# Kernel optimization log

Hardware: AMD Instinct MI355X
Metric: run time of the kernel (lower is better)

Reference implementation:

```python
import jax, jax.numpy as jnp
import numpy as np

DN = ('NCHW', 'OIHW', 'NCHW')

def conv3x3(x, w):
    return jax.lax.conv_general_dilated(x, w, (1, 1), ((1, 1), (1, 1)), dimension_numbers=DN)

def dsc(x, w1, w2):
    # DynamicSparseConv: per-sample per-channel softmax 3x3 depthwise kernel + residual
    B, C, H, W = x.shape
    pooled = x.mean(axis=(2, 3))                                  # [B, C] (AdaptiveAvgPool2d(1))
    h = jax.nn.gelu(pooled @ w1.T, approximate=False)             # [B, Cr] (1x1 conv == matmul)
    logits = (h @ w2.T).reshape(B, C, 9)                          # [B, C, 9]
    wk = jax.nn.softmax(logits, axis=2)
    # 3x3 patches: [B, C*9, H, W], feature dim ordered (C, kh, kw)
    patches = jax.lax.conv_general_dilated_patches(x, (3, 3), (1, 1), ((1, 1), (1, 1)))
    patches = patches.reshape(B, C, 9, H, W)
    out = jnp.einsum('bckhw,bck->bchw', patches, wk)
    return out + x

def pixel_shuffle(x, r):
    B, C, H, W = x.shape
    c = C // (r * r)
    return x.reshape(B, c, r, r, H, W).transpose(0, 1, 4, 2, 5, 3).reshape(B, c, H * r, W * r)

def setup_inputs() -> dict:
    key = jax.random.key(0)
    ks = jax.random.split(key, 12)
    B, C, H, W, OUT = 16, 128, 64, 64, 64
    CR = max(4, C // 8)            # 16
    RE = max(4, OUT // 8)          # 8
    s = 0.05
    return {
        'x1': jax.random.normal(ks[0], (B, C, H, W), jnp.float32),
        'x2': jax.random.normal(ks[1], (B, C, H, W), jnp.float32),
        'd1_w1': jax.random.normal(ks[2], (CR, C), jnp.float32) * s,
        'd1_w2': jax.random.normal(ks[3], (9 * C, CR), jnp.float32) * s,
        'd2_w1': jax.random.normal(ks[4], (CR, C), jnp.float32) * s,
        'd2_w2': jax.random.normal(ks[5], (9 * C, CR), jnp.float32) * s,
        'align_w': jax.random.normal(ks[6], (C, 2 * C), jnp.float32) * s,
        'up_w1': jax.random.normal(ks[7], (4 * C, C, 3, 3), jnp.float32) * s,
        'up_w2': jax.random.normal(ks[8], (OUT, C), jnp.float32) * s,
        're_w1': jax.random.normal(ks[9], (RE, OUT, 3, 3), jnp.float32) * s,
        're_w2': jax.random.normal(ks[10], (OUT, RE, 3, 3), jnp.float32) * s,
    }

def reference(x1, x2, d1_w1, d1_w2, d2_w1, d2_w2, align_w, up_w1, up_w2, re_w1, re_w2):
    def dynamic_block(x):  # shared weights for both inputs (same nn.Sequential)
        x = dsc(x, d1_w1, d1_w2)
        x = jax.nn.relu(x)
        return dsc(x, d2_w1, d2_w2)
    a = dynamic_block(x1)
    b = dynamic_block(x2)
    fused = jnp.einsum('bchw,oc->bohw', jnp.concatenate([a, b], axis=1), align_w)  # 1x1 conv
    u = conv3x3(fused, up_w1)            # [B, 4C, H, W]
    u = pixel_shuffle(u, 2)              # [B, C, 2H, 2W]
    up = jnp.einsum('bchw,oc->bohw', u, up_w2)  # [B, OUT, 2H, 2W]
    re = conv3x3(jax.nn.relu(conv3x3(up, re_w1)), re_w2)
    return up + re
```

## Files before the change

### kernel.cpp

```cpp
#include <hip/hip_runtime.h>
#include <math.h>

typedef unsigned short ushort;
typedef short bf16x8 __attribute__((ext_vector_type(8)));
typedef float f32x16 __attribute__((ext_vector_type(16)));
typedef float f32x4 __attribute__((ext_vector_type(4)));

static const size_t OFF_POOLED = 0;
static const size_t OFF_WK     = 4096;
static const size_t OFF_WT     = 40960;
static const size_t OFF_WF     = 188416;
static const size_t OFF_AW1    = 204800;
static const size_t OFF_AW2    = 209408;
static const size_t OFF_T      = 262144;
static const size_t OFF_AB     = 8650752;
static const size_t OFF_F      = 17039360;

static __device__ __forceinline__ ushort f2bf(float f) {
    unsigned int u = __builtin_bit_cast(unsigned int, f);
    u += 0x7FFF + ((u >> 16) & 1);
    return (ushort)(u >> 16);
}
static __device__ __forceinline__ float bf2f(ushort u) {
    return __builtin_bit_cast(float, ((unsigned int)u) << 16);
}

__global__ __launch_bounds__(256) void pool_both_kernel(const float* __restrict__ x1,
                                                        const float* __restrict__ x2,
                                                        float* __restrict__ pooled) {
    int bc = blockIdx.x;
    const float* x = (bc >> 11) ? x2 : x1;
    const float4* p = (const float4*)(x + (size_t)(bc & 2047) * 4096);
    float s = 0.f;
    for (int i = threadIdx.x; i < 1024; i += 256) {
        float4 v = p[i];
        s += v.x + v.y + v.z + v.w;
    }
    #pragma unroll
    for (int off = 32; off; off >>= 1) s += __shfl_down(s, off);
    __shared__ float r4[4];
    if ((threadIdx.x & 63) == 0) r4[threadIdx.x >> 6] = s;
    __syncthreads();
    if (threadIdx.x == 0) pooled[bc] = (r4[0] + r4[1] + r4[2] + r4[3]) * (1.f / 4096.f);
}

__global__ __launch_bounds__(128) void wk_kernel(const float* __restrict__ pooled,
                                                 const float* __restrict__ w1,
                                                 const float* __restrict__ w2,
                                                 float* __restrict__ wk) {
    int b = blockIdx.x;
    __shared__ float sp[128];
    __shared__ float sh[16];
    int t = threadIdx.x;
    sp[t] = pooled[b * 128 + t];
    __syncthreads();
    if (t < 16) {
        float acc = 0.f;
        #pragma unroll 4
        for (int c = 0; c < 128; c++) acc += w1[t * 128 + c] * sp[c];
        sh[t] = 0.5f * acc * (1.f + erff(acc * 0.70710678118654752f));
    }
    __syncthreads();
    float lg[9];
    float m = -INFINITY;
    #pragma unroll
    for (int k = 0; k < 9; k++) {
        float acc = 0.f;
        const float* wr = w2 + (size_t)(t * 9 + k) * 16;
        #pragma unroll
        for (int r = 0; r < 16; r++) acc += wr[r] * sh[r];
        lg[k] = acc;
        m = fmaxf(m, acc);
    }
    float se = 0.f;
    #pragma unroll
    for (int k = 0; k < 9; k++) { lg[k] = expf(lg[k] - m); se += lg[k]; }
    float inv = 1.f / se;
    #pragma unroll
    for (int k = 0; k < 9; k++) wk[(size_t)(b * 128 + t) * 9 + k] = lg[k] * inv;
}

__global__ __launch_bounds__(256) void dsc1_kernel(const float* __restrict__ x1,
                                                   const float* __restrict__ x2,
                                                   const float* __restrict__ wk,
                                                   ushort* __restrict__ y,
                                                   float* __restrict__ pooled2) {
    int bc = blockIdx.x;
    const float* xp = ((bc >> 11) ? x2 : x1) + (size_t)(bc & 2047) * 4096;
    ushort* yp = y + (size_t)bc * 4096;
    __shared__ float tile[66 * 66];
    __shared__ float r4[4];
    int t = threadIdx.x;
    for (int i = t; i < 66 * 66; i += 256) tile[i] = 0.f;
    __syncthreads();
    const float4* xp4 = (const float4*)xp;
    for (int i = t; i < 1024; i += 256) {
        float4 v = xp4[i];
        int h = i >> 4, w = (i & 15) * 4;
        float* d = &tile[(h + 1) * 66 + w + 1];
        d[0] = v.x; d[1] = v.y; d[2] = v.z; d[3] = v.w;
    }
    __syncthreads();
    float kk[9];
    #pragma unroll
    for (int k = 0; k < 9; k++) kk[k] = wk[(size_t)bc * 9 + k];
    float psum = 0.f;
    for (int i = t * 2; i < 4096; i += 512) {
        int h = i >> 6, w = i & 63;
        const float* c = &tile[h * 66 + w];
        float v0 = kk[0]*c[0] + kk[1]*c[1] + kk[2]*c[2]
                 + kk[3]*c[66] + kk[4]*c[67] + kk[5]*c[68]
                 + kk[6]*c[132] + kk[7]*c[133] + kk[8]*c[134] + c[67];
        float v1 = kk[0]*c[1] + kk[1]*c[2] + kk[2]*c[3]
                 + kk[3]*c[67] + kk[4]*c[68] + kk[5]*c[69]
                 + kk[6]*c[133] + kk[7]*c[134] + kk[8]*c[135] + c[68];
        v0 = fmaxf(v0, 0.f); v1 = fmaxf(v1, 0.f);
        psum += v0 + v1;
        ushort2 pk = {f2bf(v0), f2bf(v1)};
        *(ushort2*)&yp[i] = pk;
    }
    #pragma unroll
    for (int off = 32; off; off >>= 1) psum += __shfl_down(psum, off);
    if ((t & 63) == 0) r4[t >> 6] = psum;
    __syncthreads();
    if (t == 0) pooled2[bc] = (r4[0] + r4[1] + r4[2] + r4[3]) * (1.f / 4096.f);
}

__global__ __launch_bounds__(256) void dsc2_kernel(const ushort* __restrict__ x,
                                                   const float* __restrict__ wk,
                                                   ushort* __restrict__ y) {
    int bc = blockIdx.x;
    const ushort* xp = x + (size_t)bc * 4096;
    ushort* yp = y + (size_t)bc * 4096;
    __shared__ float tile[66 * 66];
    int t = threadIdx.x;
    for (int i = t; i < 66 * 66; i += 256) tile[i] = 0.f;
    __syncthreads();
    for (int i = t; i < 512; i += 256) {
        int4 raw = *(const int4*)&xp[i * 8];
        const ushort* u = (const ushort*)&raw;
        int h = i >> 3, w = (i & 7) * 8;
        float* d = &tile[(h + 1) * 66 + w + 1];
        #pragma unroll
        for (int j = 0; j < 8; j++) d[j] = bf2f(u[j]);
    }
    __syncthreads();
    float kk[9];
    #pragma unroll
    for (int k = 0; k < 9; k++) kk[k] = wk[(size_t)bc * 9 + k];
    for (int i = t * 2; i < 4096; i += 512) {
        int h = i >> 6, w = i & 63;
        const float* c = &tile[h * 66 + w];
        float v0 = kk[0]*c[0] + kk[1]*c[1] + kk[2]*c[2]
                 + kk[3]*c[66] + kk[4]*c[67] + kk[5]*c[68]
                 + kk[6]*c[132] + kk[7]*c[133] + kk[8]*c[134] + c[67];
        float v1 = kk[0]*c[1] + kk[1]*c[2] + kk[2]*c[3]
                 + kk[3]*c[67] + kk[4]*c[68] + kk[5]*c[69]
                 + kk[6]*c[133] + kk[7]*c[134] + kk[8]*c[135] + c[68];
        ushort2 pk = {f2bf(v0), f2bf(v1)};
        *(ushort2*)&yp[i] = pk;
    }
}

__global__ __launch_bounds__(256) void awprep_kernel(const float* __restrict__ W,
                                                     ushort* __restrict__ Wf) {
    int t = threadIdx.x;
    #pragma unroll 1
    for (int i = 0; i < 16; i++) {
        int tk = t + (i << 8);
        int step = tk >> 8, mt = (tk >> 6) & 3, lane = tk & 63;
        int o = mt * 32 + (lane & 31);
        int cb = step * 16 + (lane >> 5) * 8;
        #pragma unroll
        for (int j = 0; j < 8; j++) Wf[(size_t)tk * 8 + j] = f2bf(W[o * 256 + cb + j]);
    }
}

__global__ __launch_bounds__(256, 2) void align_mfma_kernel(const ushort* __restrict__ A,
                                                            const ushort* __restrict__ Bv,
                                                            const ushort* __restrict__ Wf,
                                                            ushort* __restrict__ F) {
    __shared__ ushort Xs[2 * 128 * 8];
    const int b = blockIdx.y;
    const int px0 = blockIdx.x << 7;
    const int tid = threadIdx.x;
    const int wave = tid >> 6, lane = tid & 63;
    const int l31 = lane & 31, half = lane >> 5;

    f32x16 acc[4];
    #pragma unroll
    for (int mt = 0; mt < 4; mt++)
        #pragma unroll
        for (int r = 0; r < 16; r++) acc[mt][r] = 0.f;

    const int cg0 = tid >> 7, pxs0 = tid & 127;
    const int bfofs = (wave * 32 + l31) * 8 + half * 1024;

    for (int step = 0; step < 16; step++) {
        const ushort* src =
            (step < 8 ? A : Bv) + (((size_t)(b * 128 + (step & 7) * 16)) << 12) + px0;
        if (step) __syncthreads();
        #pragma unroll
        for (int q = 0; q < 2; q++) {
            int cg = cg0 + q * 2, px = pxs0;
            ushort v0 = src[((size_t)(cg * 4 + 0) << 12) + px];
            ushort v1 = src[((size_t)(cg * 4 + 1) << 12) + px];
            ushort v2 = src[((size_t)(cg * 4 + 2) << 12) + px];
            ushort v3 = src[((size_t)(cg * 4 + 3) << 12) + px];
            ushort4 pk = {v0, v1, v2, v3};
            *(ushort4*)&Xs[(cg >> 1) * 1024 + px * 8 + (cg & 1) * 4] = pk;
        }
        __syncthreads();
        bf16x8 bfrag = *(const bf16x8*)&Xs[bfofs];
        const bf16x8* wf = (const bf16x8*)(Wf + ((size_t)step * 4 * 64 + lane) * 8);
        #pragma unroll
        for (int mt = 0; mt < 4; mt++)
            acc[mt] = __builtin_amdgcn_mfma_f32_32x32x16_bf16(wf[mt * 64], bfrag, acc[mt], 0, 0, 0);
    }
    ushort* fp = F + ((size_t)(b * 4096 + px0 + wave * 32 + l31)) * 128;
    #pragma unroll
    for (int mt = 0; mt < 4; mt++) {
        #pragma unroll
        for (int g = 0; g < 4; g++) {
            ushort4 pk = {f2bf(acc[mt][g * 4 + 0]), f2bf(acc[mt][g * 4 + 1]),
                          f2bf(acc[mt][g * 4 + 2]), f2bf(acc[mt][g * 4 + 3])};
            *(ushort4*)(fp + mt * 32 + half * 4 + 8 * g) = pk;
        }
    }
}

__global__ __launch_bounds__(256) void wcomb_kernel(const float* __restrict__ w1,
                                                    const float* __restrict__ w2,
                                                    ushort* __restrict__ Awt) {
    int idx = blockIdx.x * 256 + threadIdx.x;
    int j = idx & 7;
    int lane = (idx >> 3) & 63;
    int mt = (idx >> 9) & 3;
    int mh = (idx >> 11) & 1;
    int s = idx >> 12;
    int tap = s >> 3, c16 = s & 7;
    int op = mh * 128 + mt * 32 + (lane & 31);
    int cin = c16 * 16 + (lane >> 5) * 8 + j;
    int o = op >> 2, ph = op & 3;
    float acc = 0.f;
    #pragma unroll 4
    for (int c = 0; c < 128; c++)
        acc += w2[o * 128 + c] * w1[((size_t)(c * 4 + ph) * 128 + cin) * 9 + tap];
    Awt[idx] = f2bf(acc);
}

__global__ __launch_bounds__(256) void aw1prep_kernel(const float* __restrict__ w1,
                                                      ushort* __restrict__ Aw1) {
    int idx = blockIdx.x * 256 + threadIdx.x;
    if (idx >= 9216) return;
    int j = idx & 7, lane = (idx >> 3) & 63, s = idx >> 9;
    int m = lane & 15, kq = lane >> 4;
    int tap = s >> 1, ch = s & 1;
    int cin = ch * 32 + kq * 8 + j;
    float v = (m < 8) ? w1[((size_t)(m * 64 + cin)) * 9 + tap] : 0.f;
    Aw1[idx] = f2bf(v);
}

__global__ __launch_bounds__(256) void aw2prep_kernel(const float* __restrict__ w2,
                                                      ushort* __restrict__ Aw2) {
    int idx = blockIdx.x * 256 + threadIdx.x;
    if (idx >= 5120) return;
    int j = idx & 7, lane = (idx >> 3) & 63, mt = (idx >> 9) & 1, s = idx >> 10;
    int m = mt * 32 + (lane & 31), half = lane >> 5;
    int k = s * 16 + half * 8 + j;
    int tap = k >> 3, c = k & 7;
    float v = (tap < 9) ? w2[((size_t)(m * 8 + c)) * 9 + tap] : 0.f;
    Aw2[idx] = f2bf(v);
}

__global__ __launch_bounds__(256, 2) void up_mfma_kernel(const ushort* __restrict__ F,
                                                         const ushort* __restrict__ Awt,
                                                         ushort* __restrict__ U) {
    __shared__ ushort Xs[180 * 136];
    const int b = blockIdx.y;
    const int tr = blockIdx.x >> 3, tc = blockIdx.x & 7;
    const int tid = threadIdx.x;
    const int wave = tid >> 6, lane = tid & 63;
    const int l31 = lane & 31, half = lane >> 5;
    const int mh = wave >> 1, nh = wave & 1;

    for (int idx = tid; idx < 2880; idx += 256) {
        int px = idx >> 4, q = idx & 15;
        int r = px / 10, c = px - r * 10;
        int gh = tr * 16 - 1 + r, gw = tc * 8 - 1 + c;
        int4 v = {0, 0, 0, 0};
        if ((unsigned)gh < 64u && (unsigned)gw < 64u)
            v = *(const int4*)(F + ((size_t)(b * 4096 + gh * 64 + gw)) * 128 + q * 8);
        *(int4*)&Xs[px * 136 + q * 8] = v;
    }
    __syncthreads();

    f32x16 acc[4][2];
    #pragma unroll
    for (int mt = 0; mt < 4; mt++)
        #pragma unroll
        for (int nt = 0; nt < 2; nt++)
            #pragma unroll
            for (int r = 0; r < 16; r++) acc[mt][nt][r] = 0.f;

    int xb[2];
    #pragma unroll
    for (int nt = 0; nt < 2; nt++) {
        int pxl = nh * 64 + nt * 32 + l31;
        xb[nt] = ((pxl >> 3) * 10 + (pxl & 7)) * 136 + half * 8;
    }

    const ushort* abase = Awt + (size_t)(mh * 4) * 512 + lane * 8;
    bf16x8 A0[4], A1[4], AN0[4], AN1[4];
    #pragma unroll
    for (int mt = 0; mt < 4; mt++) {
        A0[mt] = *(const bf16x8*)(abase + (size_t)mt * 512);
        A1[mt] = *(const bf16x8*)(abase + 4096 + (size_t)mt * 512);
    }

    #pragma unroll 1
    for (int s = 0; s < 72; s += 2) {
        if (s + 2 < 72) {
            #pragma unroll
            for (int mt = 0; mt < 4; mt++)
                AN0[mt] = *(const bf16x8*)(abase + (size_t)(s + 2) * 4096 + mt * 512);
        }
        {
            int tap = s >> 3, c16 = s & 7;
            int ky = tap / 3, kx = tap - ky * 3;
            int xoff = (ky * 10 + kx) * 136 + c16 * 16;
            bf16x8 b0 = *(const bf16x8*)&Xs[xb[0] + xoff];
            bf16x8 b1 = *(const bf16x8*)&Xs[xb[1] + xoff];
            #pragma unroll
            for (int mt = 0; mt < 4; mt++) {
                acc[mt][0] = __builtin_amdgcn_mfma_f32_32x32x16_bf16(A0[mt], b0, acc[mt][0], 0, 0, 0);
                acc[mt][1] = __builtin_amdgcn_mfma_f32_32x32x16_bf16(A0[mt], b1, acc[mt][1], 0, 0, 0);
            }
        }
        if (s + 3 < 72) {
            #pragma unroll
            for (int mt = 0; mt < 4; mt++)
                AN1[mt] = *(const bf16x8*)(abase + (size_t)(s + 3) * 4096 + mt * 512);
        }
        {
            int s1 = s + 1;
            int tap = s1 >> 3, c16 = s1 & 7;
            int ky = tap / 3, kx = tap - ky * 3;
            int xoff = (ky * 10 + kx) * 136 + c16 * 16;
            bf16x8 b0 = *(const bf16x8*)&Xs[xb[0] + xoff];
            bf16x8 b1 = *(const bf16x8*)&Xs[xb[1] + xoff];
            #pragma unroll
            for (int mt = 0; mt < 4; mt++) {
                acc[mt][0] = __builtin_amdgcn_mfma_f32_32x32x16_bf16(A1[mt], b0, acc[mt][0], 0, 0, 0);
                acc[mt][1] = __builtin_amdgcn_mfma_f32_32x32x16_bf16(A1[mt], b1, acc[mt][1], 0, 0, 0);
            }
        }
        #pragma unroll
        for (int mt = 0; mt < 4; mt++) { A0[mt] = AN0[mt]; A1[mt] = AN1[mt]; }
    }

    const int S2 = 68;
    #pragma unroll 1
    for (int p = 0; p < 2; p++) {
        __syncthreads();
        if (nh == p) {
            #pragma unroll
            for (int nt = 0; nt < 2; nt++) {
                int pxl = nh * 64 + nt * 32 + l31;
                int rowl = pxl >> 3, coll = pxl & 7;
                int Y0 = 2 * (rowl - 8 * p), X0 = 2 * coll;
                #pragma unroll
                for (int mt = 0; mt < 4; mt++) {
                    #pragma unroll
                    for (int g = 0; g < 4; g++) {
                        int o = mh * 32 + mt * 8 + 2 * g + half;
                        #pragma unroll
                        for (int i = 0; i < 4; i++) {
                            int ry = (i >> 1), rx = i & 1;
                            Xs[((Y0 + ry) * 16 + X0 + rx) * S2 + o] =
                                f2bf(acc[mt][nt][g * 4 + i]);
                        }
                    }
                }
            }
        }
        __syncthreads();
        for (int idx = tid; idx < 4096; idx += 256) {
            int px = idx >> 4, q = idx & 15;
            ushort4 v = *(ushort4*)&Xs[px * S2 + q * 4];
            int Yg = tr * 32 + p * 16 + (px >> 4), Xg = tc * 16 + (px & 15);
            *(ushort4*)(U + ((size_t)((b * 128 + Yg) * 128 + Xg)) * 64 + q * 4) = v;
        }
    }
}

__global__ __launch_bounds__(256, 2) void re1_kernel(const ushort* __restrict__ U,
                                                     const ushort* __restrict__ Aw1,
                                                     ushort* __restrict__ R1) {
    __shared__ ushort Xs[324 * 72];
    __shared__ ushort As[18 * 64 * 8];
    const int b = blockIdx.y;
    const int ty = blockIdx.x >> 3, tx = blockIdx.x & 7;
    const int tid = threadIdx.x;
    const int wave = tid >> 6, lane = tid & 63;
    const int m16 = lane & 15, kq = lane >> 4;

    for (int idx = tid; idx < 1152; idx += 256)
        *(int4*)&As[idx * 8] = *(const int4*)(Aw1 + (size_t)idx * 8);
    for (int idx = tid; idx < 2592; idx += 256) {
        int px = idx >> 3, q = idx & 7;
        int r = px / 18, c = px - r * 18;
        int gY = ty * 16 - 1 + r, gX = tx * 16 - 1 + c;
        int4 v = {0, 0, 0, 0};
        if ((unsigned)gY < 128u && (unsigned)gX < 128u)
            v = *(const int4*)(U + ((size_t)((b * 128 + gY) * 128 + gX)) * 64 + q * 8);
        *(int4*)&Xs[px * 72 + q * 8] = v;
    }
    __syncthreads();

    f32x4 acc[4];
    #pragma unroll
    for (int nt = 0; nt < 4; nt++)
        #pragma unroll
        for (int r = 0; r < 4; r++) acc[nt][r] = 0.f;

    #pragma unroll 1
    for (int s = 0; s < 18; s++) {
        bf16x8 a = *(const bf16x8*)&As[(s * 64 + lane) * 8];
        int tap = s >> 1, ch = s & 1;
        int ky = tap / 3, kx = tap - ky * 3;
        int xo = (ky * 18 + kx) * 72 + ch * 32 + kq * 8;
        #pragma unroll
        for (int nt = 0; nt < 4; nt++) {
            int row = wave * 4 + nt;
            bf16x8 bv = *(const bf16x8*)&Xs[(row * 18 + m16) * 72 + xo];
            acc[nt] = __builtin_amdgcn_mfma_f32_16x16x32_bf16(a, bv, acc[nt], 0, 0, 0);
        }
    }
    if (kq < 2) {
        #pragma unroll
        for (int nt = 0; nt < 4; nt++) {
            int gY = ty * 16 + wave * 4 + nt, gX = tx * 16 + m16;
            ushort4 pk = {f2bf(fmaxf(acc[nt][0], 0.f)), f2bf(fmaxf(acc[nt][1], 0.f)),
                          f2bf(fmaxf(acc[nt][2], 0.f)), f2bf(fmaxf(acc[nt][3], 0.f))};
            *(ushort4*)(R1 + ((size_t)((b * 128 + gY) * 128 + gX)) * 8 + kq * 4) = pk;
        }
    }
}

__global__ __launch_bounds__(256, 2) void re2_kernel(const ushort* __restrict__ R1,
                                                     const ushort* __restrict__ U,
                                                     const ushort* __restrict__ Aw2,
                                                     float* __restrict__ out) {
    __shared__ ushort Xs[324 * 8];
    __shared__ ushort As[5 * 2 * 64 * 8];
    __shared__ ushort Us[256 * 68];
    const int b = blockIdx.y;
    const int ty = blockIdx.x >> 3, tx = blockIdx.x & 7;
    const int tid = threadIdx.x;
    const int wave = tid >> 6, lane = tid & 63;
    const int l31 = lane & 31, half = lane >> 5;

    for (int idx = tid; idx < 640; idx += 256)
        *(int4*)&As[idx * 8] = *(const int4*)(Aw2 + (size_t)idx * 8);
    for (int idx = tid; idx < 324; idx += 256) {
        int r = idx / 18, c = idx - r * 18;
        int gY = ty * 16 - 1 + r, gX = tx * 16 - 1 + c;
        int4 v = {0, 0, 0, 0};
        if ((unsigned)gY < 128u && (unsigned)gX < 128u)
            v = *(const int4*)(R1 + ((size_t)((b * 128 + gY) * 128 + gX)) * 8);
        *(int4*)&Xs[idx * 8] = v;
    }
    for (int idx = tid; idx < 2048; idx += 256) {
        int px = idx >> 3, q = idx & 7;
        int gY = ty * 16 + (px >> 4), gX = tx * 16 + (px & 15);
        const ushort* s = U + ((size_t)((b * 128 + gY) * 128 + gX)) * 64 + q * 8;
        ushort4 v0 = *(const ushort4*)s;
        ushort4 v1 = *(const ushort4*)(s + 4);
        *(ushort4*)&Us[px * 68 + q * 8] = v0;
        *(ushort4*)&Us[px * 68 + q * 8 + 4] = v1;
    }
    __syncthreads();

    f32x16 acc[2][2];
    #pragma unroll
    for (int mt = 0; mt < 2; mt++)
        #pragma unroll
        for (int nt = 0; nt < 2; nt++)
            #pragma unroll
            for (int r = 0; r < 16; r++) acc[mt][nt][r] = 0.f;

    #pragma unroll
    for (int s = 0; s < 5; s++) {
        bf16x8 a0 = *(const bf16x8*)&As[((s * 2 + 0) * 64 + lane) * 8];
        bf16x8 a1 = *(const bf16x8*)&As[((s * 2 + 1) * 64 + lane) * 8];
        int t = 2 * s + half;
        if (t > 8) t = 8;
        int ky = t / 3, kx = t - ky * 3;
        #pragma unroll
        for (int nt = 0; nt < 2; nt++) {
            int pxl = wave * 64 + nt * 32 + l31;
            int row = pxl >> 4, col = pxl & 15;
            bf16x8 bv = *(const bf16x8*)&Xs[((row + ky) * 18 + col + kx) * 8];
            acc[0][nt] = __builtin_amdgcn_mfma_f32_32x32x16_bf16(a0, bv, acc[0][nt], 0, 0, 0);
            acc[1][nt] = __builtin_amdgcn_mfma_f32_32x32x16_bf16(a1, bv, acc[1][nt], 0, 0, 0);
        }
    }
    #pragma unroll
    for (int mt = 0; mt < 2; mt++) {
        #pragma unroll
        for (int nt = 0; nt < 2; nt++) {
            int pxl = wave * 64 + nt * 32 + l31;
            int gY = ty * 16 + (pxl >> 4), gX = tx * 16 + (pxl & 15);
            #pragma unroll
            for (int r = 0; r < 16; r++) {
                int o = mt * 32 + (r & 3) + 8 * (r >> 2) + 4 * half;
                float v = acc[mt][nt][r] + bf2f(Us[pxl * 68 + o]);
                out[((size_t)(b * 64 + o) * 128 + gY) * 128 + gX] = v;
            }
        }
    }
}

extern "C" void kernel_launch(void* const* d_in, const int* in_sizes, int n_in,
                              void* d_out, int out_size, void* d_ws, size_t ws_size,
                              hipStream_t stream) {
    const float* x1      = (const float*)d_in[0];
    const float* x2      = (const float*)d_in[1];
    const float* d1_w1   = (const float*)d_in[2];
    const float* d1_w2   = (const float*)d_in[3];
    const float* d2_w1   = (const float*)d_in[4];
    const float* d2_w2   = (const float*)d_in[5];
    const float* align_w = (const float*)d_in[6];
    const float* up_w1   = (const float*)d_in[7];
    const float* up_w2   = (const float*)d_in[8];
    const float* re_w1   = (const float*)d_in[9];
    const float* re_w2   = (const float*)d_in[10];
    float* out = (float*)d_out;
    float* ws  = (float*)d_ws;

    float*  pooled = ws + OFF_POOLED;
    float*  wkb    = ws + OFF_WK;
    ushort* Awt    = (ushort*)(ws + OFF_WT);
    ushort* Wf     = (ushort*)(ws + OFF_WF);
    ushort* Aw1    = (ushort*)(ws + OFF_AW1);
    ushort* Aw2    = (ushort*)(ws + OFF_AW2);
    ushort* bufT   = (ushort*)(ws + OFF_T);
    ushort* R1     = (ushort*)(ws + OFF_T);
    ushort* bufAB  = (ushort*)(ws + OFF_AB);
    ushort* bufU   = (ushort*)(ws + OFF_AB);
    ushort* F      = (ushort*)(ws + OFF_F);

    wcomb_kernel<<<1152, 256, 0, stream>>>(up_w1, up_w2, Awt);
    awprep_kernel<<<1, 256, 0, stream>>>(align_w, Wf);
    aw1prep_kernel<<<36, 256, 0, stream>>>(re_w1, Aw1);
    aw2prep_kernel<<<20, 256, 0, stream>>>(re_w2, Aw2);

    pool_both_kernel<<<4096, 256, 0, stream>>>(x1, x2, pooled);
    wk_kernel<<<32, 128, 0, stream>>>(pooled, d1_w1, d1_w2, wkb);
    dsc1_kernel<<<4096, 256, 0, stream>>>(x1, x2, wkb, bufT, pooled);
    wk_kernel<<<32, 128, 0, stream>>>(pooled, d2_w1, d2_w2, wkb);
    dsc2_kernel<<<4096, 256, 0, stream>>>(bufT, wkb, bufAB);

    align_mfma_kernel<<<dim3(32, 16), 256, 0, stream>>>(bufAB, bufAB + 8388608, Wf, F);
    up_mfma_kernel<<<dim3(32, 16), 256, 0, stream>>>(F, Awt, bufU);
    re1_kernel<<<dim3(64, 16), 256, 0, stream>>>(bufU, Aw1, R1);
    re2_kernel<<<dim3(64, 16), 256, 0, stream>>>(R1, bufU, Aw2, out);
}
```

Before: 359.5 us.

## Fuse dynamic-kernel computation into dsc kernels and split up-conv output channels

Removes the two small wk_kernel launches and instead recomputes, inside each dsc block, the gelu MLP hidden vector and that channel's 9 softmax weights from the pooled vector. The up_mfma kernel now splits its output channels across two blocks, doubling the grid. Each block holds half the accumulators and uses an XOR-swizzled unpadded LDS layout for the input tile, and the launch bound is raised to 3 blocks per CU. The cost is redundant per-block MLP work (16x128 dot products per block) and the input tile being loaded twice in the up conv.

Measured after the change: 368.0 us. 2.3% more time.

```diff
diff --git a/kernel.cpp b/kernel.cpp
--- a/kernel.cpp
+++ b/kernel.cpp
@@ -44,45 +44,11 @@
     if (threadIdx.x == 0) pooled[bc] = (r4[0] + r4[1] + r4[2] + r4[3]) * (1.f / 4096.f);
 }
 
-__global__ __launch_bounds__(128) void wk_kernel(const float* __restrict__ pooled,
-                                                 const float* __restrict__ w1,
-                                                 const float* __restrict__ w2,
-                                                 float* __restrict__ wk) {
-    int b = blockIdx.x;
-    __shared__ float sp[128];
-    __shared__ float sh[16];
-    int t = threadIdx.x;
-    sp[t] = pooled[b * 128 + t];
-    __syncthreads();
-    if (t < 16) {
-        float acc = 0.f;
-        #pragma unroll 4
-        for (int c = 0; c < 128; c++) acc += w1[t * 128 + c] * sp[c];
-        sh[t] = 0.5f * acc * (1.f + erff(acc * 0.70710678118654752f));
-    }
-    __syncthreads();
-    float lg[9];
-    float m = -INFINITY;
-    #pragma unroll
-    for (int k = 0; k < 9; k++) {
-        float acc = 0.f;
-        const float* wr = w2 + (size_t)(t * 9 + k) * 16;
-        #pragma unroll
-        for (int r = 0; r < 16; r++) acc += wr[r] * sh[r];
-        lg[k] = acc;
-        m = fmaxf(m, acc);
-    }
-    float se = 0.f;
-    #pragma unroll
-    for (int k = 0; k < 9; k++) { lg[k] = expf(lg[k] - m); se += lg[k]; }
-    float inv = 1.f / se;
-    #pragma unroll
-    for (int k = 0; k < 9; k++) wk[(size_t)(b * 128 + t) * 9 + k] = lg[k] * inv;
-}
-
 __global__ __launch_bounds__(256) void dsc1_kernel(const float* __restrict__ x1,
                                                    const float* __restrict__ x2,
-                                                   const float* __restrict__ wk,
+                                                   const float* __restrict__ pooled,
+                                                   const float* __restrict__ w1,
+                                                   const float* __restrict__ w2,
                                                    ushort* __restrict__ y,
                                                    float* __restrict__ pooled2) {
     int bc = blockIdx.x;
@@ -90,9 +56,19 @@
     ushort* yp = y + (size_t)bc * 4096;
     __shared__ float tile[66 * 66];
     __shared__ float r4[4];
+    __shared__ float sp[128];
+    __shared__ float sh[16];
+    __shared__ float lgs[9];
     int t = threadIdx.x;
+    if (t < 128) sp[t] = pooled[(bc >> 7) * 128 + t];
     for (int i = t; i < 66 * 66; i += 256) tile[i] = 0.f;
     __syncthreads();
+    if (t < 16) {
+        float a = 0.f;
+        #pragma unroll 4
+        for (int c = 0; c < 128; c++) a += w1[t * 128 + c] * sp[c];
+        sh[t] = 0.5f * a * (1.f + erff(a * 0.70710678118654752f));
+    }
     const float4* xp4 = (const float4*)xp;
     for (int i = t; i < 1024; i += 256) {
         float4 v = xp4[i];
@@ -101,9 +77,26 @@
         d[0] = v.x; d[1] = v.y; d[2] = v.z; d[3] = v.w;
     }
     __syncthreads();
+    if (t < 9) {
+        float a = 0.f;
+        const float* wr = w2 + (size_t)((bc & 127) * 9 + t) * 16;
+        #pragma unroll
+        for (int r = 0; r < 16; r++) a += wr[r] * sh[r];
+        lgs[t] = a;
+    }
+    __syncthreads();
     float kk[9];
-    #pragma unroll
-    for (int k = 0; k < 9; k++) kk[k] = wk[(size_t)bc * 9 + k];
+    {
+        float m = -INFINITY;
+        #pragma unroll
+        for (int k = 0; k < 9; k++) m = fmaxf(m, lgs[k]);
+        float se = 0.f;
+        #pragma unroll
+        for (int k = 0; k < 9; k++) { kk[k] = expf(lgs[k] - m); se += kk[k]; }
+        float inv = 1.f / se;
+        #pragma unroll
+        for (int k = 0; k < 9; k++) kk[k] *= inv;
+    }
     float psum = 0.f;
     for (int i = t * 2; i < 4096; i += 512) {
         int h = i >> 6, w = i & 63;
@@ -127,15 +120,27 @@
 }
 
 __global__ __launch_bounds__(256) void dsc2_kernel(const ushort* __restrict__ x,
-                                                   const float* __restrict__ wk,
+                                                   const float* __restrict__ pooled,
+                                                   const float* __restrict__ w1,
+                                                   const float* __restrict__ w2,
                                                    ushort* __restrict__ y) {
     int bc = blockIdx.x;
     const ushort* xp = x + (size_t)bc * 4096;
     ushort* yp = y + (size_t)bc * 4096;
     __shared__ float tile[66 * 66];
+    __shared__ float sp[128];
+    __shared__ float sh[16];
+    __shared__ float lgs[9];
     int t = threadIdx.x;
+    if (t < 128) sp[t] = pooled[(bc >> 7) * 128 + t];
     for (int i = t; i < 66 * 66; i += 256) tile[i] = 0.f;
     __syncthreads();
+    if (t < 16) {
+        float a = 0.f;
+        #pragma unroll 4
+        for (int c = 0; c < 128; c++) a += w1[t * 128 + c] * sp[c];
+        sh[t] = 0.5f * a * (1.f + erff(a * 0.70710678118654752f));
+    }
     for (int i = t; i < 512; i += 256) {
         int4 raw = *(const int4*)&xp[i * 8];
         const ushort* u = (const ushort*)&raw;
@@ -145,9 +150,26 @@
         for (int j = 0; j < 8; j++) d[j] = bf2f(u[j]);
     }
     __syncthreads();
+    if (t < 9) {
+        float a = 0.f;
+        const float* wr = w2 + (size_t)((bc & 127) * 9 + t) * 16;
+        #pragma unroll
+        for (int r = 0; r < 16; r++) a += wr[r] * sh[r];
+        lgs[t] = a;
+    }
+    __syncthreads();
     float kk[9];
-    #pragma unroll
-    for (int k = 0; k < 9; k++) kk[k] = wk[(size_t)bc * 9 + k];
+    {
+        float m = -INFINITY;
+        #pragma unroll
+        for (int k = 0; k < 9; k++) m = fmaxf(m, lgs[k]);
+        float se = 0.f;
+        #pragma unroll
+        for (int k = 0; k < 9; k++) { kk[k] = expf(lgs[k] - m); se += kk[k]; }
+        float inv = 1.f / se;
+        #pragma unroll
+        for (int k = 0; k < 9; k++) kk[k] *= inv;
+    }
     for (int i = t * 2; i < 4096; i += 512) {
         int h = i >> 6, w = i & 63;
         const float* c = &tile[h * 66 + w];
@@ -273,16 +295,18 @@
     Aw2[idx] = f2bf(v);
 }
 
-__global__ __launch_bounds__(256, 2) void up_mfma_kernel(const ushort* __restrict__ F,
+__global__ __launch_bounds__(256, 3) void up_mfma_kernel(const ushort* __restrict__ F,
                                                          const ushort* __restrict__ Awt,
                                                          ushort* __restrict__ U) {
-    __shared__ ushort Xs[180 * 136];
+    __shared__ ushort Xs[180 * 128];
     const int b = blockIdx.y;
-    const int tr = blockIdx.x >> 3, tc = blockIdx.x & 7;
+    const int oh = blockIdx.x & 1;
+    const int tile = blockIdx.x >> 1;
+    const int tr = tile >> 3, tc = tile & 7;
     const int tid = threadIdx.x;
     const int wave = tid >> 6, lane = tid & 63;
     const int l31 = lane & 31, half = lane >> 5;
-    const int mh = wave >> 1, nh = wave & 1;
+    const int mh2 = wave >> 1, nh = wave & 1;
 
     for (int idx = tid; idx < 2880; idx += 256) {
         int px = idx >> 4, q = idx & 15;
@@ -291,29 +315,29 @@
         int4 v = {0, 0, 0, 0};
         if ((unsigned)gh < 64u && (unsigned)gw < 64u)
             v = *(const int4*)(F + ((size_t)(b * 4096 + gh * 64 + gw)) * 128 + q * 8);
-        *(int4*)&Xs[px * 136 + q * 8] = v;
-    }
-    __syncthreads();
-
-    f32x16 acc[4][2];
-    #pragma unroll
-    for (int mt = 0; mt < 4; mt++)
+        *(int4*)&Xs[px * 128 + ((q ^ (px & 7)) << 3)] = v;
+    }
+    __syncthreads();
+
+    f32x16 acc[2][2];
+    #pragma unroll
+    for (int mt = 0; mt < 2; mt++)
         #pragma unroll
         for (int nt = 0; nt < 2; nt++)
             #pragma unroll
             for (int r = 0; r < 16; r++) acc[mt][nt][r] = 0.f;
 
-    int xb[2];
+    int xpos[2];
     #pragma unroll
     for (int nt = 0; nt < 2; nt++) {
         int pxl = nh * 64 + nt * 32 + l31;
-        xb[nt] = ((pxl >> 3) * 10 + (pxl & 7)) * 136 + half * 8;
-    }
-
-    const ushort* abase = Awt + (size_t)(mh * 4) * 512 + lane * 8;
-    bf16x8 A0[4], A1[4], AN0[4], AN1[4];
-    #pragma unroll
-    for (int mt = 0; mt < 4; mt++) {
+        xpos[nt] = (pxl >> 3) * 10 + (pxl & 7);
+    }
+
+    const ushort* abase = Awt + (size_t)(oh * 4 + mh2 * 2) * 512 + lane * 8;
+    bf16x8 A0[2], A1[2], AN0[2], AN1[2];
+    #pragma unroll
+    for (int mt = 0; mt < 2; mt++) {
         A0[mt] = *(const bf16x8*)(abase + (size_t)mt * 512);
         A1[mt] = *(const bf16x8*)(abase + 4096 + (size_t)mt * 512);
     }
@@ -322,44 +346,48 @@
     for (int s = 0; s < 72; s += 2) {
         if (s + 2 < 72) {
             #pragma unroll
-            for (int mt = 0; mt < 4; mt++)
+            for (int mt = 0; mt < 2; mt++)
                 AN0[mt] = *(const bf16x8*)(abase + (size_t)(s + 2) * 4096 + mt * 512);
         }
         {
             int tap = s >> 3, c16 = s & 7;
             int ky = tap / 3, kx = tap - ky * 3;
-            int xoff = (ky * 10 + kx) * 136 + c16 * 16;
-            bf16x8 b0 = *(const bf16x8*)&Xs[xb[0] + xoff];
-            bf16x8 b1 = *(const bf16x8*)&Xs[xb[1] + xoff];
-            #pragma unroll
-            for (int mt = 0; mt < 4; mt++) {
+            int koff = ky * 10 + kx;
+            int qq = c16 * 2 + half;
+            int p0 = xpos[0] + koff, p1 = xpos[1] + koff;
+            bf16x8 b0 = *(const bf16x8*)&Xs[p0 * 128 + ((qq ^ (p0 & 7)) << 3)];
+            bf16x8 b1 = *(const bf16x8*)&Xs[p1 * 128 + ((qq ^ (p1 & 7)) << 3)];
+            #pragma unroll
+            for (int mt = 0; mt < 2; mt++) {
                 acc[mt][0] = __builtin_amdgcn_mfma_f32_32x32x16_bf16(A0[mt], b0, acc[mt][0], 0, 0, 0);
                 acc[mt][1] = __builtin_amdgcn_mfma_f32_32x32x16_bf16(A0[mt], b1, acc[mt][1], 0, 0, 0);
             }
         }
         if (s + 3 < 72) {
             #pragma unroll
-            for (int mt = 0; mt < 4; mt++)
+            for (int mt = 0; mt < 2; mt++)
                 AN1[mt] = *(const bf16x8*)(abase + (size_t)(s + 3) * 4096 + mt * 512);
         }
         {
             int s1 = s + 1;
             int tap = s1 >> 3, c16 = s1 & 7;
             int ky = tap / 3, kx = tap - ky * 3;
-            int xoff = (ky * 10 + kx) * 136 + c16 * 16;
-            bf16x8 b0 = *(const bf16x8*)&Xs[xb[0] + xoff];
-            bf16x8 b1 = *(const bf16x8*)&Xs[xb[1] + xoff];
-            #pragma unroll
-            for (int mt = 0; mt < 4; mt++) {
+            int koff = ky * 10 + kx;
+            int qq = c16 * 2 + half;
+            int p0 = xpos[0] + koff, p1 = xpos[1] + koff;
+            bf16x8 b0 = *(const bf16x8*)&Xs[p0 * 128 + ((qq ^ (p0 & 7)) << 3)];
+            bf16x8 b1 = *(const bf16x8*)&Xs[p1 * 128 + ((qq ^ (p1 & 7)) << 3)];
+            #pragma unroll
+            for (int mt = 0; mt < 2; mt++) {
                 acc[mt][0] = __builtin_amdgcn_mfma_f32_32x32x16_bf16(A1[mt], b0, acc[mt][0], 0, 0, 0);
                 acc[mt][1] = __builtin_amdgcn_mfma_f32_32x32x16_bf16(A1[mt], b1, acc[mt][1], 0, 0, 0);
             }
         }
         #pragma unroll
-        for (int mt = 0; mt < 4; mt++) { A0[mt] = AN0[mt]; A1[mt] = AN1[mt]; }
-    }
-
-    const int S2 = 68;
+        for (int mt = 0; mt < 2; mt++) { A0[mt] = AN0[mt]; A1[mt] = AN1[mt]; }
+    }
+
+    const int S2 = 36;
     #pragma unroll 1
     for (int p = 0; p < 2; p++) {
         __syncthreads();
@@ -370,10 +398,10 @@
                 int rowl = pxl >> 3, coll = pxl & 7;
                 int Y0 = 2 * (rowl - 8 * p), X0 = 2 * coll;
                 #pragma unroll
-                for (int mt = 0; mt < 4; mt++) {
+                for (int mt = 0; mt < 2; mt++) {
                     #pragma unroll
                     for (int g = 0; g < 4; g++) {
-                        int o = mh * 32 + mt * 8 + 2 * g + half;
+                        int o = mh2 * 16 + mt * 8 + 2 * g + half;
                         #pragma unroll
                         for (int i = 0; i < 4; i++) {
                             int ry = (i >> 1), rx = i & 1;
@@ -385,11 +413,11 @@
             }
         }
         __syncthreads();
-        for (int idx = tid; idx < 4096; idx += 256) {
-            int px = idx >> 4, q = idx & 15;
+        for (int idx = tid; idx < 2048; idx += 256) {
+            int px = idx >> 3, q = idx & 7;
             ushort4 v = *(ushort4*)&Xs[px * S2 + q * 4];
             int Yg = tr * 32 + p * 16 + (px >> 4), Xg = tc * 16 + (px & 15);
-            *(ushort4*)(U + ((size_t)((b * 128 + Yg) * 128 + Xg)) * 64 + q * 4) = v;
+            *(ushort4*)(U + ((size_t)((b * 128 + Yg) * 128 + Xg)) * 64 + oh * 32 + q * 4) = v;
         }
     }
 }
@@ -539,8 +567,8 @@
     float* out = (float*)d_out;
     float* ws  = (float*)d_ws;
 
-    float*  pooled = ws + OFF_POOLED;
-    float*  wkb    = ws + OFF_WK;
+    float*  pooled  = ws + OFF_POOLED;
+    float*  pooled2 = ws + OFF_WK;
     ushort* Awt    = (ushort*)(ws + OFF_WT);
     ushort* Wf     = (ushort*)(ws + OFF_WF);
     ushort* Aw1    = (ushort*)(ws + OFF_AW1);
@@ -557,13 +585,11 @@
     aw2prep_kernel<<<20, 256, 0, stream>>>(re_w2, Aw2);
 
     pool_both_kernel<<<4096, 256, 0, stream>>>(x1, x2, pooled);
-    wk_kernel<<<32, 128, 0, stream>>>(pooled, d1_w1, d1_w2, wkb);
-    dsc1_kernel<<<4096, 256, 0, stream>>>(x1, x2, wkb, bufT, pooled);
-    wk_kernel<<<32, 128, 0, stream>>>(pooled, d2_w1, d2_w2, wkb);
-    dsc2_kernel<<<4096, 256, 0, stream>>>(bufT, wkb, bufAB);
+    dsc1_kernel<<<4096, 256, 0, stream>>>(x1, x2, pooled, d1_w1, d1_w2, bufT, pooled2);
+    dsc2_kernel<<<4096, 256, 0, stream>>>(bufT, pooled2, d2_w1, d2_w2, bufAB);
 
     align_mfma_kernel<<<dim3(32, 16), 256, 0, stream>>>(bufAB, bufAB + 8388608, Wf, F);
-    up_mfma_kernel<<<dim3(32, 16), 256, 0, stream>>>(F, Awt, bufU);
+    up_mfma_kernel<<<dim3(64, 16), 256, 0, stream>>>(F, Awt, bufU);
     re1_kernel<<<dim3(64, 16), 256, 0, stream>>>(bufU, Aw1, R1);
     re2_kernel<<<dim3(64, 16), 256, 0, stream>>>(R1, bufU, Aw2, out);
 }
```

## Permute fused weight rows for direct U stores and swizzle input LDS tile

Applied to the files above, without the earlier changes.

Reorders the rows of the combined up-conv/1x1 weight matrix so each MFMA output lane holds contiguous output channels for one pixel-shuffle phase. This lets the epilogue write bf16 results straight to global memory as 16-byte vectors, with no LDS staging pass and its two barriers. The input tile in LDS switches from padded rows to an XOR-swizzled layout to avoid bank conflicts, and the B fragments are now software-prefetched one step ahead alongside A. Correctness depends on the row permutation matching the 32x32 MFMA accumulator lane layout exactly.

Result: faster. 339.6 us (-5.5%).

```diff
diff --git a/kernel.cpp b/kernel.cpp
--- a/kernel.cpp
+++ b/kernel.cpp
@@ -3,6 +3,7 @@
 
 typedef unsigned short ushort;
 typedef short bf16x8 __attribute__((ext_vector_type(8)));
+typedef ushort us8 __attribute__((ext_vector_type(8)));
 typedef float f32x16 __attribute__((ext_vector_type(16)));
 typedef float f32x4 __attribute__((ext_vector_type(4)));
 
@@ -239,13 +240,14 @@
     int mh = (idx >> 11) & 1;
     int s = idx >> 12;
     int tap = s >> 3, c16 = s & 7;
-    int op = mh * 128 + mt * 32 + (lane & 31);
+    int arow = lane & 31;
+    int o_sem = (mt & 1) * 32 + (arow & 3) + 4 * ((arow >> 3) & 3) + 16 * ((arow >> 2) & 1);
+    int ph = 2 * mh + (mt >> 1);
     int cin = c16 * 16 + (lane >> 5) * 8 + j;
-    int o = op >> 2, ph = op & 3;
     float acc = 0.f;
     #pragma unroll 4
     for (int c = 0; c < 128; c++)
-        acc += w2[o * 128 + c] * w1[((size_t)(c * 4 + ph) * 128 + cin) * 9 + tap];
+        acc += w2[o_sem * 128 + c] * w1[((size_t)(c * 4 + ph) * 128 + cin) * 9 + tap];
     Awt[idx] = f2bf(acc);
 }
 
@@ -276,7 +278,7 @@
 __global__ __launch_bounds__(256, 2) void up_mfma_kernel(const ushort* __restrict__ F,
                                                          const ushort* __restrict__ Awt,
                                                          ushort* __restrict__ U) {
-    __shared__ ushort Xs[180 * 136];
+    __shared__ ushort Xs[180 * 128];
     const int b = blockIdx.y;
     const int tr = blockIdx.x >> 3, tc = blockIdx.x & 7;
     const int tid = threadIdx.x;
@@ -291,7 +293,7 @@
         int4 v = {0, 0, 0, 0};
         if ((unsigned)gh < 64u && (unsigned)gw < 64u)
             v = *(const int4*)(F + ((size_t)(b * 4096 + gh * 64 + gw)) * 128 + q * 8);
-        *(int4*)&Xs[px * 136 + q * 8] = v;
+        *(int4*)&Xs[px * 128 + ((q ^ (px & 7)) << 3)] = v;
     }
     __syncthreads();
 
@@ -303,93 +305,77 @@
             #pragma unroll
             for (int r = 0; r < 16; r++) acc[mt][nt][r] = 0.f;
 
-    int xb[2];
+    int xpos[2];
     #pragma unroll
     for (int nt = 0; nt < 2; nt++) {
         int pxl = nh * 64 + nt * 32 + l31;
-        xb[nt] = ((pxl >> 3) * 10 + (pxl & 7)) * 136 + half * 8;
+        xpos[nt] = (pxl >> 3) * 10 + (pxl & 7);
     }
 
     const ushort* abase = Awt + (size_t)(mh * 4) * 512 + lane * 8;
-    bf16x8 A0[4], A1[4], AN0[4], AN1[4];
+
+    #define LDB(ss, nt) ({                                                   \
+        int tap_ = (ss) >> 3, c16_ = (ss) & 7;                               \
+        int ky_ = (tap_ * 11) >> 5;                      \
+        int kx_ = tap_ - ky_ * 3;                                            \
+        int p_ = xpos[nt] + ky_ * 10 + kx_;                                  \
+        int qq_ = c16_ * 2 + half;                                           \
+        *(const bf16x8*)&Xs[p_ * 128 + ((qq_ ^ (p_ & 7)) << 3)];             \
+    })
+
+    bf16x8 A0[4], A1[4], B0[2], B1[2];
     #pragma unroll
     for (int mt = 0; mt < 4; mt++) {
         A0[mt] = *(const bf16x8*)(abase + (size_t)mt * 512);
         A1[mt] = *(const bf16x8*)(abase + 4096 + (size_t)mt * 512);
     }
+    B0[0] = LDB(0, 0); B0[1] = LDB(0, 1);
+    B1[0] = LDB(1, 0); B1[1] = LDB(1, 1);
 
     #pragma unroll 1
     for (int s = 0; s < 72; s += 2) {
+        #pragma unroll
+        for (int mt = 0; mt < 4; mt++) {
+            acc[mt][0] = __builtin_amdgcn_mfma_f32_32x32x16_bf16(A0[mt], B0[0], acc[mt][0], 0, 0, 0);
+            acc[mt][1] = __builtin_amdgcn_mfma_f32_32x32x16_bf16(A0[mt], B0[1], acc[mt][1], 0, 0, 0);
+        }
         if (s + 2 < 72) {
             #pragma unroll
             for (int mt = 0; mt < 4; mt++)
-                AN0[mt] = *(const bf16x8*)(abase + (size_t)(s + 2) * 4096 + mt * 512);
-        }
-        {
-            int tap = s >> 3, c16 = s & 7;
-            int ky = tap / 3, kx = tap - ky * 3;
-            int xoff = (ky * 10 + kx) * 136 + c16 * 16;
-            bf16x8 b0 = *(const bf16x8*)&Xs[xb[0] + xoff];
-            bf16x8 b1 = *(const bf16x8*)&Xs[xb[1] + xoff];
-            #pragma unroll
-            for (int mt = 0; mt < 4; mt++) {
-                acc[mt][0] = __builtin_amdgcn_mfma_f32_32x32x16_bf16(A0[mt], b0, acc[mt][0], 0, 0, 0);
-                acc[mt][1] = __builtin_amdgcn_mfma_f32_32x32x16_bf16(A0[mt], b1, acc[mt][1], 0, 0, 0);
-            }
+                A0[mt] = *(const bf16x8*)(abase + (size_t)(s + 2) * 4096 + mt * 512);
+            B0[0] = LDB(s + 2, 0); B0[1] = LDB(s + 2, 1);
+        }
+        #pragma unroll
+        for (int mt = 0; mt < 4; mt++) {
+            acc[mt][0] = __builtin_amdgcn_mfma_f32_32x32x16_bf16(A1[mt], B1[0], acc[mt][0], 0, 0, 0);
+            acc[mt][1] = __builtin_amdgcn_mfma_f32_32x32x16_bf16(A1[mt], B1[1], acc[mt][1], 0, 0, 0);
         }
         if (s + 3 < 72) {
             #pragma unroll
             for (int mt = 0; mt < 4; mt++)
-                AN1[mt] = *(const bf16x8*)(abase + (size_t)(s + 3) * 4096 + mt * 512);
-        }
-        {
-            int s1 = s + 1;
-            int tap = s1 >> 3, c16 = s1 & 7;
-            int ky = tap / 3, kx = tap - ky * 3;
-            int xoff = (ky * 10 + kx) * 136 + c16 * 16;
-            bf16x8 b0 = *(const bf16x8*)&Xs[xb[0] + xoff];
-            bf16x8 b1 = *(const bf16x8*)&Xs[xb[1] + xoff];
+                A1[mt] = *(const bf16x8*)(abase + (size_t)(s + 3) * 4096 + mt * 512);
+            B1[0] = LDB(s + 3, 0); B1[1] = LDB(s + 3, 1);
+        }
+    }
+    #undef LDB
+
+    #pragma unroll
+    for (int nt = 0; nt < 2; nt++) {
+        int pxl = nh * 64 + nt * 32 + l31;
+        int Y = 2 * (tr * 16 + (pxl >> 3)) + mh;
+        int X = 2 * (tc * 8 + (pxl & 7));
+        #pragma unroll
+        for (int mt = 0; mt < 4; mt++) {
+            ushort* up = U + ((size_t)((b * 128 + Y) * 128 + X + (mt >> 1))) * 64
+                       + (mt & 1) * 32 + half * 16;
+            us8 p0, p1;
             #pragma unroll
-            for (int mt = 0; mt < 4; mt++) {
-                acc[mt][0] = __builtin_amdgcn_mfma_f32_32x32x16_bf16(A1[mt], b0, acc[mt][0], 0, 0, 0);
-                acc[mt][1] = __builtin_amdgcn_mfma_f32_32x32x16_bf16(A1[mt], b1, acc[mt][1], 0, 0, 0);
+            for (int i = 0; i < 8; i++) {
+                p0[i] = f2bf(acc[mt][nt][i]);
+                p1[i] = f2bf(acc[mt][nt][8 + i]);
             }
-        }
-        #pragma unroll
-        for (int mt = 0; mt < 4; mt++) { A0[mt] = AN0[mt]; A1[mt] = AN1[mt]; }
-    }
-
-    const int S2 = 68;
-    #pragma unroll 1
-    for (int p = 0; p < 2; p++) {
-        __syncthreads();
-        if (nh == p) {
-            #pragma unroll
-            for (int nt = 0; nt < 2; nt++) {
-                int pxl = nh * 64 + nt * 32 + l31;
-                int rowl = pxl >> 3, coll = pxl & 7;
-                int Y0 = 2 * (rowl - 8 * p), X0 = 2 * coll;
-                #pragma unroll
-                for (int mt = 0; mt < 4; mt++) {
-                    #pragma unroll
-                    for (int g = 0; g < 4; g++) {
-                        int o = mh * 32 + mt * 8 + 2 * g + half;
-                        #pragma unroll
-                        for (int i = 0; i < 4; i++) {
-                            int ry = (i >> 1), rx = i & 1;
-                            Xs[((Y0 + ry) * 16 + X0 + rx) * S2 + o] =
-                                f2bf(acc[mt][nt][g * 4 + i]);
-                        }
-                    }
-                }
-            }
-        }
-        __syncthreads();
-        for (int idx = tid; idx < 4096; idx += 256) {
-            int px = idx >> 4, q = idx & 15;
-            ushort4 v = *(ushort4*)&Xs[px * S2 + q * 4];
-            int Yg = tr * 32 + p * 16 + (px >> 4), Xg = tc * 16 + (px & 15);
-            *(ushort4*)(U + ((size_t)((b * 128 + Yg) * 128 + Xg)) * 64 + q * 4) = v;
+            *(us8*)up = p0;
+            *(us8*)(up + 8) = p1;
         }
     }
 }
```
